# Kernel optimization log

Hardware: AMD Instinct MI355X
Metric: run time of the kernel (lower is better)

The kernel has to match this reference:

```python
import jax, jax.numpy as jnp
import numpy as np

N, K, D = 65536, 4096, 64


def setup_inputs() -> dict:
    key = jax.random.key(0)
    kx, ke = jax.random.split(key)
    x = jax.random.normal(kx, (N, D), dtype=jnp.float32)
    embed = jax.random.normal(ke, (1, K, D), dtype=jnp.float32)
    return {"x": x, "embed": embed}


def reference(x, embed):
    # Faithful to EuclideanCodebook.forward quantization path:
    #   dist = cdist(flatten, embed, p=2)**2 ; argmin ; one_hot @ embed
    xf = x.astype(jnp.float32)            # [N, D]
    e = embed[0]                          # [K, D]
    # squared euclidean distance via expansion (== cdist(...).pow(2))
    x_sq = jnp.sum(xf * xf, axis=-1, keepdims=True)        # [N, 1]
    e_sq = jnp.sum(e * e, axis=-1)                          # [K]
    dist = jnp.maximum(x_sq + e_sq[None, :] - 2.0 * (xf @ e.T), 0.0)  # [N, K]
    embed_ind = jnp.argmin(dist, axis=-1)                   # [N]
    # one_hot @ embed is exactly a row gather of the codebook
    quantize = e[embed_ind]                                 # [N, D]
    return quantize, embed_ind[None, :]                     # embed_ind kept as [1, N] like torch
```

## Files before the change

### kernel.cpp

```cpp
#include <hip/hip_runtime.h>
#include <math.h>

#define N_ROWS 65536
#define K_CODES 4096
#define DIM 64
#define NTILES (K_CODES / 32)
#define MARGIN 0.01f

typedef __attribute__((ext_vector_type(8))) short bf16x8;
typedef __attribute__((ext_vector_type(16))) float f32x16;

__device__ inline unsigned short f2bf_rne(float f) {
    unsigned u = __float_as_uint(f);
    return (unsigned short)((u + 0x7FFFu + ((u >> 16) & 1u)) >> 16);
}
__device__ inline float bf2f(unsigned short s) {
    return __uint_as_float(((unsigned)s) << 16);
}

__global__ __launch_bounds__(256) void pack_e(const float* __restrict__ embed,
                                              short* __restrict__ e_pk,
                                              float* __restrict__ esq,
                                              int* __restrict__ count) {
    __shared__ float lds_f[2048];
    const int tile = blockIdx.x;
    const int t = threadIdx.x;
    if (tile == 0 && t == 0) *count = 0;
    const float4* src = (const float4*)(embed + (size_t)tile * 2048);
    ((float4*)lds_f)[t] = src[t];
    ((float4*)lds_f)[t + 256] = src[t + 256];
    __syncthreads();
    const int l = t & 63, ks = t >> 6;
    const int base = (l & 31) * 64 + ks * 16 + (l >> 5) * 8;
    bf16x8 vh, vl;
#pragma unroll
    for (int j = 0; j < 8; ++j) {
        float v = lds_f[base + j];
        unsigned short h = f2bf_rne(v);
        vh[j] = (short)h;
        vl[j] = (short)f2bf_rne(v - bf2f(h));
    }
    *(bf16x8*)(e_pk + (size_t)tile * 4096 + t * 8) = vh;
    *(bf16x8*)(e_pk + (size_t)tile * 4096 + 2048 + t * 8) = vl;
    if (t < 32) {
        float s = 0.f;
#pragma unroll
        for (int d = 0; d < 64; ++d) { float v = lds_f[t * 64 + d]; s = fmaf(v, v, s); }
        esq[tile * 32 + t] = s;
    }
}

__global__ __launch_bounds__(256, 2) void vq_main(const float* __restrict__ x,
                                                  const short* __restrict__ e_pk,
                                                  const float* __restrict__ esq,
                                                  int* __restrict__ idxf,
                                                  int* __restrict__ list,
                                                  int* __restrict__ count) {
    __shared__ __align__(16) char lds[2][8192];
    const int tid = threadIdx.x;
    const int wid = tid >> 6;
    const int l = tid & 63;
    const int col = l & 31;
    const int g = l >> 5;
    const int rowbase = blockIdx.x * 128 + wid * 32;

    const float* xrow = x + (size_t)(rowbase + col) * DIM;
    bf16x8 ah[4], al[4];
#pragma unroll
    for (int ks = 0; ks < 4; ++ks) {
        const float* p = xrow + ks * 16 + g * 8;
#pragma unroll
        for (int j = 0; j < 8; ++j) {
            float v = p[j];
            unsigned short h = f2bf_rne(v);
            ah[ks][j] = (short)h;
            al[ks][j] = (short)f2bf_rne(v - bf2f(h));
        }
    }

    float b1[16], b2[16];
    int i1[16];
#pragma unroll
    for (int i = 0; i < 16; ++i) { b1[i] = 3.0e38f; b2[i] = 3.0e38f; i1[i] = 0; }

    auto stage = [&](int t, int b) {
        const char* gsrc = (const char*)e_pk + (size_t)t * 8192 + tid * 16;
        __builtin_amdgcn_global_load_lds(
            (const __attribute__((address_space(1))) void*)gsrc,
            (__attribute__((address_space(3))) void*)(&lds[b][wid * 1024]), 16, 0, 0);
        __builtin_amdgcn_global_load_lds(
            (const __attribute__((address_space(1))) void*)(gsrc + 4096),
            (__attribute__((address_space(3))) void*)(&lds[b][4096 + wid * 1024]), 16, 0, 0);
    };

    stage(0, 0);
    asm volatile("s_waitcnt vmcnt(0)" ::: "memory");
    __syncthreads();

    for (int t = 0; t < NTILES; ++t) {
        const int cur = t & 1;
        if (t + 1 < NTILES) stage(t + 1, cur ^ 1);
        const float esq_v = esq[t * 32 + col];
        const int cidx = t * 32 + col;

        f32x16 acc;
#pragma unroll
        for (int i = 0; i < 16; ++i) acc[i] = 0.f;

#pragma unroll
        for (int ks = 0; ks < 4; ++ks) {
            const bf16x8 bh = *(const bf16x8*)(&lds[cur][(ks * 64 + l) * 16]);
            const bf16x8 bl = *(const bf16x8*)(&lds[cur][4096 + (ks * 64 + l) * 16]);
            acc = __builtin_amdgcn_mfma_f32_32x32x16_bf16(ah[ks], bh, acc, 0, 0, 0);
            acc = __builtin_amdgcn_mfma_f32_32x32x16_bf16(ah[ks], bl, acc, 0, 0, 0);
            acc = __builtin_amdgcn_mfma_f32_32x32x16_bf16(al[ks], bh, acc, 0, 0, 0);
        }

#pragma unroll
        for (int i = 0; i < 16; ++i) {
            float key = fmaf(-2.0f, acc[i], esq_v);
            bool lt = key < b1[i];
            float sel = lt ? b1[i] : key;
            b2[i] = fminf(b2[i], sel);
            b1[i] = lt ? key : b1[i];
            i1[i] = lt ? cidx : i1[i];
        }

        asm volatile("s_waitcnt vmcnt(0)" ::: "memory");
        __syncthreads();
    }

#pragma unroll
    for (int i = 0; i < 16; ++i) {
#pragma unroll
        for (int m = 1; m <= 16; m <<= 1) {
            float ob1 = __shfl_xor(b1[i], m);
            float ob2 = __shfl_xor(b2[i], m);
            int oi = __shfl_xor(i1[i], m);
            float nb2 = fminf(fmaxf(b1[i], ob1), fminf(b2[i], ob2));
            bool take = ob1 < b1[i];
            b1[i] = take ? ob1 : b1[i];
            i1[i] = take ? oi : i1[i];
            b2[i] = nb2;
        }
        if (col == 0) {
            int row = rowbase + (i & 3) + 8 * (i >> 2) + 4 * g;
            idxf[row] = i1[i];
            if (b2[i] - b1[i] < MARGIN) {
                int p = atomicAdd(count, 1);
                list[p] = row;
            }
        }
    }
}

__global__ __launch_bounds__(256) void vq_rescore(const float* __restrict__ x,
                                                  const float* __restrict__ embed,
                                                  const float* __restrict__ esq,
                                                  int* __restrict__ idxf,
                                                  const int* __restrict__ list,
                                                  const int* __restrict__ count) {
    __shared__ float xs[64];
    __shared__ float sk[256];
    __shared__ int si[256];
    const int tid = threadIdx.x;
    const int n = *count;
    for (int f = blockIdx.x; f < n; f += gridDim.x) {
        const int row = list[f];
        if (tid < 16) ((float4*)xs)[tid] = ((const float4*)(x + (size_t)row * DIM))[tid];
        __syncthreads();
        float best = 3.0e38f;
        int bi = 0;
        for (int i = 0; i < 16; ++i) {
            int c = tid + (i << 8);
            const float* e = embed + (size_t)c * DIM;
            float d0 = 0, d1 = 0, d2 = 0, d3 = 0;
#pragma unroll
            for (int d = 0; d < 64; d += 4) {
                d0 = fmaf(xs[d + 0], e[d + 0], d0);
                d1 = fmaf(xs[d + 1], e[d + 1], d1);
                d2 = fmaf(xs[d + 2], e[d + 2], d2);
                d3 = fmaf(xs[d + 3], e[d + 3], d3);
            }
            float key = fmaf(-2.f, (d0 + d1) + (d2 + d3), esq[c]);
            if (key < best) { best = key; bi = c; }
        }
        sk[tid] = best; si[tid] = bi;
        __syncthreads();
        for (int s = 128; s > 0; s >>= 1) {
            if (tid < s) {
                float ok = sk[tid + s]; int oi = si[tid + s];
                if (ok < sk[tid] || (ok == sk[tid] && oi < si[tid])) { sk[tid] = ok; si[tid] = oi; }
            }
            __syncthreads();
        }
        if (tid == 0) idxf[row] = si[0];
        __syncthreads();
    }
}

__global__ __launch_bounds__(256) void vq_gather(const float* __restrict__ embed,
                                                 const int* __restrict__ idxf,
                                                 float* __restrict__ out_q,
                                                 float* __restrict__ out_ind) {
    int t = blockIdx.x * 256 + threadIdx.x;
    int r = t >> 3, q = t & 7;
    int c = idxf[r];
    const float4* src = (const float4*)(embed + (size_t)c * DIM + q * 8);
    float4* dst = (float4*)(out_q + (size_t)r * DIM + q * 8);
    dst[0] = src[0];
    dst[1] = src[1];
    if (q == 0) out_ind[r] = (float)c;
}

extern "C" void kernel_launch(void* const* d_in, const int* in_sizes, int n_in,
                              void* d_out, int out_size, void* d_ws, size_t ws_size,
                              hipStream_t stream) {
    const float* x = (const float*)d_in[0];
    const float* embed = (const float*)d_in[1];
    float* out = (float*)d_out;

    char* ws = (char*)d_ws;
    short* e_pk = (short*)ws;
    float* esq = (float*)(ws + (1 << 20));
    int* idxf = (int*)(ws + (1 << 20) + (16 << 10));
    int* list = (int*)(ws + (1 << 20) + (16 << 10) + (256 << 10));
    int* count = (int*)(ws + (1 << 20) + (16 << 10) + (512 << 10));

    pack_e<<<K_CODES / 32, 256, 0, stream>>>(embed, e_pk, esq, count);
    vq_main<<<N_ROWS / 128, 256, 0, stream>>>(x, e_pk, esq, idxf, list, count);
    vq_rescore<<<512, 256, 0, stream>>>(x, embed, esq, idxf, list, count);
    vq_gather<<<N_ROWS * 8 / 256, 256, 0, stream>>>(embed, idxf, out,
                                                    out + (size_t)N_ROWS * DIM);
}
```

Baseline: 172.1 us.

## Split codebook into two chunks per row block and merge in gather kernel

The codebook scan is split across two blocks per row group, and each block writes its per-row best, second-best and index to workspace. A new merge-and-gather kernel combines the two partial results and flags near-ties for rescoring; the rescore kernel then writes its outputs directly. The distance key is folded into the MFMA accumulator by initialising it with -0.5*||e||^2 and tracking a maximum, with the second-best updated by med3. The launch-bounds occupancy hint is raised and the tie margin is rescaled to match the halved key. In exchange the change adds partial-result workspace traffic and duplicates the per-block x loading and conversion.

```diff
diff --git a/kernel.cpp b/kernel.cpp
--- a/kernel.cpp
+++ b/kernel.cpp
@@ -3,9 +3,11 @@
 
 #define N_ROWS 65536
 #define K_CODES 4096
+#define NTILES_TOTAL (K_CODES / 32)
+#define K_CHUNKS 2
+#define NTILES (NTILES_TOTAL / K_CHUNKS)
 #define DIM 64
-#define NTILES (K_CODES / 32)
-#define MARGIN 0.01f
+#define ACC_MARGIN 0.005f
 
 typedef __attribute__((ext_vector_type(8))) short bf16x8;
 typedef __attribute__((ext_vector_type(16))) float f32x16;
@@ -21,6 +23,7 @@
 __global__ __launch_bounds__(256) void pack_e(const float* __restrict__ embed,
                                               short* __restrict__ e_pk,
                                               float* __restrict__ esq,
+                                              float* __restrict__ esqn,
                                               int* __restrict__ count) {
     __shared__ float lds_f[2048];
     const int tile = blockIdx.x;
@@ -47,22 +50,26 @@
 #pragma unroll
         for (int d = 0; d < 64; ++d) { float v = lds_f[t * 64 + d]; s = fmaf(v, v, s); }
         esq[tile * 32 + t] = s;
-    }
-}
-
-__global__ __launch_bounds__(256, 2) void vq_main(const float* __restrict__ x,
+        esqn[tile * 32 + t] = -0.5f * s;
+    }
+}
+
+__global__ __launch_bounds__(256, 4) void vq_main(const float* __restrict__ x,
                                                   const short* __restrict__ e_pk,
-                                                  const float* __restrict__ esq,
-                                                  int* __restrict__ idxf,
-                                                  int* __restrict__ list,
-                                                  int* __restrict__ count) {
+                                                  const float* __restrict__ esqn,
+                                                  float* __restrict__ b1s,
+                                                  float* __restrict__ b2s,
+                                                  int* __restrict__ i1s) {
     __shared__ __align__(16) char lds[2][8192];
     const int tid = threadIdx.x;
     const int wid = tid >> 6;
     const int l = tid & 63;
     const int col = l & 31;
     const int g = l >> 5;
-    const int rowbase = blockIdx.x * 128 + wid * 32;
+    const int kc = blockIdx.x & (K_CHUNKS - 1);
+    const int rg = blockIdx.x >> 1;
+    const int rowbase = rg * 128 + wid * 32;
+    const int tile0 = kc * NTILES;
 
     const float* xrow = x + (size_t)(rowbase + col) * DIM;
     bf16x8 ah[4], al[4];
@@ -81,10 +88,10 @@
     float b1[16], b2[16];
     int i1[16];
 #pragma unroll
-    for (int i = 0; i < 16; ++i) { b1[i] = 3.0e38f; b2[i] = 3.0e38f; i1[i] = 0; }
+    for (int i = 0; i < 16; ++i) { b1[i] = -3.0e38f; b2[i] = -3.0e38f; i1[i] = 0; }
 
     auto stage = [&](int t, int b) {
-        const char* gsrc = (const char*)e_pk + (size_t)t * 8192 + tid * 16;
+        const char* gsrc = (const char*)e_pk + (size_t)(tile0 + t) * 8192 + tid * 16;
         __builtin_amdgcn_global_load_lds(
             (const __attribute__((address_space(1))) void*)gsrc,
             (__attribute__((address_space(3))) void*)(&lds[b][wid * 1024]), 16, 0, 0);
@@ -100,12 +107,12 @@
     for (int t = 0; t < NTILES; ++t) {
         const int cur = t & 1;
         if (t + 1 < NTILES) stage(t + 1, cur ^ 1);
-        const float esq_v = esq[t * 32 + col];
-        const int cidx = t * 32 + col;
+        const float esqn_v = esqn[(tile0 + t) * 32 + col];
+        const int cidx = (tile0 + t) * 32 + col;
 
         f32x16 acc;
 #pragma unroll
-        for (int i = 0; i < 16; ++i) acc[i] = 0.f;
+        for (int i = 0; i < 16; ++i) acc[i] = esqn_v;
 
 #pragma unroll
         for (int ks = 0; ks < 4; ++ks) {
@@ -118,12 +125,11 @@
 
 #pragma unroll
         for (int i = 0; i < 16; ++i) {
-            float key = fmaf(-2.0f, acc[i], esq_v);
-            bool lt = key < b1[i];
-            float sel = lt ? b1[i] : key;
-            b2[i] = fminf(b2[i], sel);
-            b1[i] = lt ? key : b1[i];
-            i1[i] = lt ? cidx : i1[i];
+            float val = acc[i];
+            bool gt = val > b1[i];
+            b2[i] = __builtin_amdgcn_fmed3f(val, b1[i], b2[i]);
+            b1[i] = fmaxf(val, b1[i]);
+            i1[i] = gt ? cidx : i1[i];
         }
 
         asm volatile("s_waitcnt vmcnt(0)" ::: "memory");
@@ -137,19 +143,47 @@
             float ob1 = __shfl_xor(b1[i], m);
             float ob2 = __shfl_xor(b2[i], m);
             int oi = __shfl_xor(i1[i], m);
-            float nb2 = fminf(fmaxf(b1[i], ob1), fminf(b2[i], ob2));
-            bool take = ob1 < b1[i];
+            float nb2 = fmaxf(fminf(b1[i], ob1), fmaxf(b2[i], ob2));
+            bool take = ob1 > b1[i];
             b1[i] = take ? ob1 : b1[i];
             i1[i] = take ? oi : i1[i];
             b2[i] = nb2;
         }
         if (col == 0) {
             int row = rowbase + (i & 3) + 8 * (i >> 2) + 4 * g;
-            idxf[row] = i1[i];
-            if (b2[i] - b1[i] < MARGIN) {
-                int p = atomicAdd(count, 1);
-                list[p] = row;
-            }
+            b1s[(size_t)kc * N_ROWS + row] = b1[i];
+            b2s[(size_t)kc * N_ROWS + row] = b2[i];
+            i1s[(size_t)kc * N_ROWS + row] = i1[i];
+        }
+    }
+}
+
+__global__ __launch_bounds__(256) void vq_merge_gather(const float* __restrict__ embed,
+                                                       const float* __restrict__ b1s,
+                                                       const float* __restrict__ b2s,
+                                                       const int* __restrict__ i1s,
+                                                       float* __restrict__ out_q,
+                                                       float* __restrict__ out_ind,
+                                                       int* __restrict__ list,
+                                                       int* __restrict__ count) {
+    int t = blockIdx.x * 256 + threadIdx.x;
+    int r = t >> 3, q = t & 7;
+    float ab1 = b1s[r], bb1 = b1s[N_ROWS + r];
+    float ab2 = b2s[r], bb2 = b2s[N_ROWS + r];
+    int ai = i1s[r], bi = i1s[N_ROWS + r];
+    bool take = bb1 > ab1;
+    int idx = take ? bi : ai;
+    float m1 = fmaxf(ab1, bb1);
+    float m2 = fmaxf(fminf(ab1, bb1), fmaxf(ab2, bb2));
+    const float4* src = (const float4*)(embed + (size_t)idx * DIM + q * 8);
+    float4* dst = (float4*)(out_q + (size_t)r * DIM + q * 8);
+    dst[0] = src[0];
+    dst[1] = src[1];
+    if (q == 0) {
+        out_ind[r] = (float)idx;
+        if (m1 - m2 < ACC_MARGIN) {
+            int p = atomicAdd(count, 1);
+            list[p] = r;
         }
     }
 }
@@ -157,9 +191,10 @@
 __global__ __launch_bounds__(256) void vq_rescore(const float* __restrict__ x,
                                                   const float* __restrict__ embed,
                                                   const float* __restrict__ esq,
-                                                  int* __restrict__ idxf,
                                                   const int* __restrict__ list,
-                                                  const int* __restrict__ count) {
+                                                  const int* __restrict__ count,
+                                                  float* __restrict__ out_q,
+                                                  float* __restrict__ out_ind) {
     __shared__ float xs[64];
     __shared__ float sk[256];
     __shared__ int si[256];
@@ -194,23 +229,13 @@
             }
             __syncthreads();
         }
-        if (tid == 0) idxf[row] = si[0];
-        __syncthreads();
-    }
-}
-
-__global__ __launch_bounds__(256) void vq_gather(const float* __restrict__ embed,
-                                                 const int* __restrict__ idxf,
-                                                 float* __restrict__ out_q,
-                                                 float* __restrict__ out_ind) {
-    int t = blockIdx.x * 256 + threadIdx.x;
-    int r = t >> 3, q = t & 7;
-    int c = idxf[r];
-    const float4* src = (const float4*)(embed + (size_t)c * DIM + q * 8);
-    float4* dst = (float4*)(out_q + (size_t)r * DIM + q * 8);
-    dst[0] = src[0];
-    dst[1] = src[1];
-    if (q == 0) out_ind[r] = (float)c;
+        if (tid == 0) out_ind[row] = (float)si[0];
+        if (tid < 16) {
+            const float4* src = (const float4*)(embed + (size_t)si[0] * DIM);
+            ((float4*)(out_q + (size_t)row * DIM))[tid] = src[tid];
+        }
+        __syncthreads();
+    }
 }
 
 extern "C" void kernel_launch(void* const* d_in, const int* in_sizes, int n_in,
@@ -219,17 +244,22 @@
     const float* x = (const float*)d_in[0];
     const float* embed = (const float*)d_in[1];
     float* out = (float*)d_out;
+    float* out_ind = out + (size_t)N_ROWS * DIM;
 
     char* ws = (char*)d_ws;
     short* e_pk = (short*)ws;
-    float* esq = (float*)(ws + (1 << 20));
-    int* idxf = (int*)(ws + (1 << 20) + (16 << 10));
-    int* list = (int*)(ws + (1 << 20) + (16 << 10) + (256 << 10));
-    int* count = (int*)(ws + (1 << 20) + (16 << 10) + (512 << 10));
-
-    pack_e<<<K_CODES / 32, 256, 0, stream>>>(embed, e_pk, esq, count);
-    vq_main<<<N_ROWS / 128, 256, 0, stream>>>(x, e_pk, esq, idxf, list, count);
-    vq_rescore<<<512, 256, 0, stream>>>(x, embed, esq, idxf, list, count);
-    vq_gather<<<N_ROWS * 8 / 256, 256, 0, stream>>>(embed, idxf, out,
-                                                    out + (size_t)N_ROWS * DIM);
-}
+    size_t off = 1 << 20;
+    float* esq = (float*)(ws + off);  off += 16 << 10;
+    float* esqn = (float*)(ws + off); off += 16 << 10;
+    float* b1s = (float*)(ws + off);  off += (size_t)K_CHUNKS * N_ROWS * 4;
+    float* b2s = (float*)(ws + off);  off += (size_t)K_CHUNKS * N_ROWS * 4;
+    int* i1s = (int*)(ws + off);      off += (size_t)K_CHUNKS * N_ROWS * 4;
+    int* list = (int*)(ws + off);     off += (size_t)N_ROWS * 4;
+    int* count = (int*)(ws + off);
+
+    pack_e<<<NTILES_TOTAL, 256, 0, stream>>>(embed, e_pk, esq, esqn, count);
+    vq_main<<<(N_ROWS / 128) * K_CHUNKS, 256, 0, stream>>>(x, e_pk, esqn, b1s, b2s, i1s);
+    vq_merge_gather<<<N_ROWS * 8 / 256, 256, 0, stream>>>(embed, b1s, b2s, i1s,
+                                                          out, out_ind, list, count);
+    vq_rescore<<<512, 256, 0, stream>>>(x, embed, esq, list, count, out, out_ind);
+}
```

After: 161.4 us. 1.07x faster.
